# Kernel optimization log

Measured on AMD Instinct MI355X. Metric: run time of the kernel, lower is better.

## Reference

```python
import jax, jax.numpy as jnp
import numpy as np

N = 100000      # nodes
E = 3200000     # edges (avg degree 32)
F_IN = 512
HID = 256
CLS = 64


def _linear_init(k, fan_in, fan_out):
    lim = 1.0 / np.sqrt(fan_in)
    kw, kb = jax.random.split(k)
    W = jax.random.uniform(kw, (fan_in, fan_out), jnp.float32, -lim, lim)
    b = jax.random.uniform(kb, (fan_out,), jnp.float32, -lim, lim)
    return W, b


def setup_inputs() -> dict:
    key = jax.random.key(0)
    ks = jax.random.split(key, 8)
    x = jax.random.normal(ks[0], (N, F_IN), jnp.float32)
    edge_src = jax.random.randint(ks[1], (E,), 0, N, jnp.int32)
    off = jax.random.randint(ks[2], (E,), 1, N, jnp.int32)
    edge_dst = ((edge_src + off) % N).astype(jnp.int32)  # no self loops
    Wm0, bm0 = _linear_init(ks[3], F_IN, HID)
    Wv0, bv0 = _linear_init(ks[4], F_IN, HID)
    Wm1, bm1 = _linear_init(ks[5], HID, CLS)
    Wv1, bv1 = _linear_init(ks[6], HID, CLS)
    sample = jax.random.normal(ks[7], (N, CLS), jnp.float32)
    return dict(x=x, Wm0=Wm0, bm0=bm0, Wv0=Wv0, bv0=bv0,
                Wm1=Wm1, bm1=bm1, Wv1=Wv1, bv1=bv1,
                sample=sample, edge_src=edge_src, edge_dst=edge_dst)


def reference(x, Wm0, bm0, Wv0, bv0, Wm1, bm1, Wv1, bv1, sample, edge_src, edge_dst):
    n = x.shape[0]
    loops = jnp.arange(n, dtype=edge_src.dtype)
    src = jnp.concatenate([edge_src, loops])  # fill_diag(adj, 1.0)
    dst = jnp.concatenate([edge_dst, loops])
    ones = jnp.ones(src.shape[0], x.dtype)
    deg = jax.ops.segment_sum(ones, src, num_segments=n)
    dis = jnp.where(deg > 0, deg ** -0.5, 0.0)   # D^-0.5
    di = jnp.where(deg > 0, 1.0 / deg, 0.0)      # D^-1
    w0 = dis[src] * dis[dst]                      # adj0 = D^-0.5 A D^-0.5
    w1 = di[src] * di[dst]                        # adj1 = D^-1  A D^-1

    def spmm(w, m):  # (adj @ m) with edge weights w
        return jax.ops.segment_sum(w[:, None] * m[dst], src, num_segments=n)

    # layer 0 (initial=True): no aggregation, dropout off (eval)
    mean = jax.nn.elu(x @ Wm0 + bm0)
    var = jax.nn.relu(x @ Wv0 + bv0)
    # layer 1: variance-attention + dual SpMM
    mean = jax.nn.elu(mean @ Wm1 + bm1)
    var = jax.nn.relu(var @ Wv1 + bv1) + 1e-6
    attn = jnp.exp(-var)
    mean = spmm(w0, mean * attn)
    var = spmm(w1, var * attn * attn)

    out = mean + sample * jnp.sqrt(var)
    return jax.nn.log_softmax(out, axis=-1)
```

## Files before the change

kernel.cpp:

```cpp
#include <hip/hip_runtime.h>
#include <cstdint>
#include <cstddef>


typedef _Float16 h8 __attribute__((ext_vector_type(8)));
typedef _Float16 h2 __attribute__((ext_vector_type(2)));
typedef float f32x4 __attribute__((ext_vector_type(4)));
typedef unsigned int uint32;

#define BSHIFT 7
#define NCHUNK 256

static __device__ __forceinline__ float elu_f(float z) {
  return z > 0.f ? z : expm1f(z);
}

static __device__ __forceinline__ void gload16(const void* g, void* l) {
  __builtin_amdgcn_global_load_lds(
      (__attribute__((address_space(1))) void*)g,
      (__attribute__((address_space(3))) void*)l, 16, 0, 0);
}

static __device__ __forceinline__ h8 cvt8(float4 a, float4 b) {
  return h8{(_Float16)a.x, (_Float16)a.y, (_Float16)a.z, (_Float16)a.w,
            (_Float16)b.x, (_Float16)b.y, (_Float16)b.z, (_Float16)b.w};
}

__global__ __launch_bounds__(256) void histprep_k(
    const int* __restrict__ esrc, int E, int chunk, int* __restrict__ h, int NB,
    const float* __restrict__ Wm0, const float* __restrict__ Wv0,
    const float* __restrict__ Wm1, const float* __restrict__ Wv1,
    _Float16* __restrict__ W1t, _Float16* __restrict__ W2t) {
  int t = threadIdx.x;
  if (blockIdx.x < NCHUNK) {
    __shared__ int sh[1024];
    for (int i = t; i < NB; i += 256) sh[i] = 0;
    __syncthreads();
    int e0 = blockIdx.x * chunk;
    int e1 = min(e0 + chunk, E);
    for (int e = e0 + t; e < e1; e += 256) atomicAdd(&sh[esrc[e] >> BSHIFT], 1);
    __syncthreads();
    for (int i = t; i < NB; i += 256) h[blockIdx.x * NB + i] = sh[i];
  } else {
    int idx = (blockIdx.x - NCHUNK) * 256 + t;
    if (idx < 512 * 512) {
      int n = idx >> 9, k = idx & 511;
      float v = (n < 256) ? Wm0[k * 256 + n] : Wv0[k * 256 + (n - 256)];
      W1t[idx] = (_Float16)v;
    }
    if (idx < 128 * 512) {
      int n = idx >> 9, k = idx & 511;
      float v = 0.f;
      if (n < 64) { if (k < 256) v = Wm1[k * 64 + n]; }
      else        { if (k >= 256) v = Wv1[(k - 256) * 64 + (n - 64)]; }
      W2t[idx] = (_Float16)v;
    }
  }
}

__global__ __launch_bounds__(256) void btotal_k(const int* __restrict__ h,
                                                int* __restrict__ tot, int NB) {
  int b = blockIdx.x, t = threadIdx.x;
  int v = h[t * NB + b];
#pragma unroll
  for (int off = 32; off; off >>= 1) v += __shfl_xor(v, off, 64);
  __shared__ int sw[4];
  if ((t & 63) == 0) sw[t >> 6] = v;
  __syncthreads();
  if (t == 0) tot[b] = sw[0] + sw[1] + sw[2] + sw[3];
}

__global__ __launch_bounds__(1024) void boff2_k(const int* __restrict__ tot,
                                                int* __restrict__ h,
                                                int* __restrict__ base, int NB) {
  __shared__ int sh[1024];
  __shared__ int bbs;
  int b = blockIdx.x, t = threadIdx.x;
  int v = (t < NB) ? tot[t] : 0;
  sh[t] = v;
  __syncthreads();
  for (int off = 1; off < 1024; off <<= 1) {
    int add = (t >= off) ? sh[t - off] : 0;
    __syncthreads();
    sh[t] += add;
    __syncthreads();
  }
  if (b == 0) {
    if (t < NB) base[t] = sh[t] - v;
    if (t == 0) base[NB] = sh[NB - 1];
  }
  if (t == 0) bbs = (b > 0) ? sh[b - 1] : 0;
  __syncthreads();
  int hv = (t < 256) ? h[t * NB + b] : 0;
  __syncthreads();
  if (t < 256) sh[t] = hv;
  __syncthreads();
  for (int off = 1; off < 256; off <<= 1) {
    int add = (t >= off && t < 256) ? sh[t - off] : 0;
    __syncthreads();
    if (t < 256) sh[t] += add;
    __syncthreads();
  }
  if (t < 256) h[t * NB + b] = bbs + sh[t] - hv;
}

__global__ __launch_bounds__(256) void bscatter_k(
    const int* __restrict__ esrc, const int* __restrict__ edst, int E, int chunk,
    const int* __restrict__ h, uint32* __restrict__ pairs, int NB) {
  __shared__ int lcur[1024];
  int t = threadIdx.x;
  for (int i = t; i < NB; i += 256) lcur[i] = h[blockIdx.x * NB + i];
  __syncthreads();
  int e0 = blockIdx.x * chunk;
  int e1 = min(e0 + chunk, E);
  for (int e = e0 + t; e < e1; e += 256) {
    int s = esrc[e], d = edst[e];
    int pos = atomicAdd(&lcur[s >> BSHIFT], 1);
    pairs[pos] = ((uint32)(s & 127) << 25) | (uint32)d;
  }
}

__global__ __launch_bounds__(256) void countN_k(
    const uint32* __restrict__ pairs, const int* __restrict__ base,
    int* __restrict__ cnt, float2* __restrict__ dd, int n) {
  __shared__ int c128[128];
  int b = blockIdx.x, t = threadIdx.x;
  if (t < 128) c128[t] = 0;
  __syncthreads();
  int lo = base[b], hi = base[b + 1];
  for (int i = lo + t; i < hi; i += 256) atomicAdd(&c128[pairs[i] >> 25], 1);
  __syncthreads();
  if (t < 128) {
    int node = b * 128 + t;
    if (node < n) {
      int c = c128[t];
      cnt[node] = c;
      float d = (float)(c + 1);
      dd[node] = make_float2(rsqrtf(d), 1.f / d);
    }
  }
}

__global__ __launch_bounds__(256) void partC_k(
    const uint32* __restrict__ pairs, const int* __restrict__ base,
    const int* __restrict__ rs, int* __restrict__ csr, int n) {
  __shared__ int lcur[128];
  int b = blockIdx.x, t = threadIdx.x;
  if (t < 128) {
    int node = b * 128 + t;
    lcur[t] = (node < n) ? rs[node] : 0;
  }
  __syncthreads();
  int lo = base[b], hi = base[b + 1];
  for (int i = lo + t; i < hi; i += 256) {
    uint32 p = pairs[i];
    int pos = atomicAdd(&lcur[p >> 25], 1);
    csr[pos] = (int)(p & 0x1FFFFFFu);
  }
}

__global__ void scan1_k(const int* __restrict__ cnt, int* __restrict__ excl,
                        int* __restrict__ bsum, int n) {
  __shared__ int sh[256];
  int t = threadIdx.x, idx = blockIdx.x * 256 + t;
  int v = (idx < n) ? ((cnt[idx] + 3) & ~3) : 0;
  sh[t] = v;
  __syncthreads();
  for (int off = 1; off < 256; off <<= 1) {
    int add = (t >= off) ? sh[t - off] : 0;
    __syncthreads();
    sh[t] += add;
    __syncthreads();
  }
  if (idx < n) excl[idx] = sh[t] - v;
  if (t == 255) bsum[blockIdx.x] = sh[255];
}

__global__ __launch_bounds__(512) void scan3m_k(int* __restrict__ excl,
                                                const int* __restrict__ bsum,
                                                int nb, int n) {
  __shared__ int sh[512];
  int t = threadIdx.x;
  int v = (t < nb) ? bsum[t] : 0;
  sh[t] = v;
  __syncthreads();
  for (int off = 1; off < 512; off <<= 1) {
    int add = (t >= off) ? sh[t - off] : 0;
    __syncthreads();
    sh[t] += add;
    __syncthreads();
  }
  int idx = blockIdx.x * 512 + t;
  if (idx < n) {
    int k = idx >> 8;
    excl[idx] += (k > 0) ? sh[k - 1] : 0;
  }
}

__global__ __launch_bounds__(256) void gemm1d_k(
    const float* __restrict__ A, const _Float16* __restrict__ Bt,
    const float* __restrict__ b0, const float* __restrict__ b1,
    _Float16* __restrict__ out, int M, int mtiles) {
  __shared__ __align__(16) unsigned char ldsb[36864];

  const int sg = blockIdx.x >> 5, loc = blockIdx.x & 31;
  const int nt = loc >> 3, mtl = loc & 7;
  const int mt = sg * 8 + mtl;
  if (mt >= mtiles) return;
  const int m0 = mt * 128, n0 = nt * 128;
  const int t = threadIdx.x;
  const int lane = t & 63;
  const int wave = t >> 6;
  const int wm = wave >> 1, wn = wave & 1;
  const int lr = lane & 15, quad = lane >> 4;

  const int ra = t >> 3;
  const int asw = ((t & 7) ^ (ra & 7)) << 2;

  const _Float16* bbase = Bt + (size_t)(n0 + wn * 64 + lr) * 512 + quad * 8;

  f32x4 acc[4][4] = {};

  auto stageA = [&](int b, int kt) {
#pragma unroll
    for (int i = 0; i < 4; i++) {
      const float* src = A + (size_t)min(m0 + i * 32 + ra, M - 1) * 512 + kt + asw;
      gload16(src, ldsb + b * 16384 + i * 4096 + t * 16);
    }
  };

  stageA(0, 0);
  __syncthreads();

  int cur = 0;
  const int zA = lr & 7;
  for (int kt = 0; kt < 512; kt += 32) {
    h8 bf[4];
#pragma unroll
    for (int j = 0; j < 4; j++)
      bf[j] = *(const h8*)(bbase + (size_t)j * 16 * 512 + kt);
    if (kt + 32 < 512) stageA(cur ^ 1, kt + 32);
    const unsigned char* Ab = ldsb + cur * 16384;
    h8 af[4];
#pragma unroll
    for (int i = 0; i < 4; i++) {
      int R = wm * 64 + i * 16 + lr;
      const float4 a0 = *(const float4*)(Ab + R * 128 + (((2 * quad) ^ zA) << 4));
      const float4 a1 = *(const float4*)(Ab + R * 128 + (((2 * quad + 1) ^ zA) << 4));
      af[i] = cvt8(a0, a1);
    }
#pragma unroll
    for (int i = 0; i < 4; i++)
#pragma unroll
      for (int j = 0; j < 4; j++)
        acc[i][j] = __builtin_amdgcn_mfma_f32_16x16x32_f16(af[i], bf[j], acc[i][j], 0, 0, 0);
    __syncthreads();
    cur ^= 1;
  }

  _Float16* lt = (_Float16*)ldsb;
#pragma unroll
  for (int j = 0; j < 4; j++) {
    int gc = n0 + wn * 64 + j * 16 + lr;
    float bj = (gc < 256) ? b0[gc] : b1[gc - 256];
#pragma unroll
    for (int i = 0; i < 4; i++) {
#pragma unroll
      for (int r = 0; r < 4; r++) {
        float z = acc[i][j][r] + bj;
        float v = (gc < 256) ? elu_f(z) : fmaxf(z, 0.f);
        lt[(wm * 64 + i * 16 + quad * 4 + r) * 136 + wn * 64 + j * 16 + lr] = (_Float16)v;
      }
    }
  }
  __syncthreads();
  {
    const int row = t >> 1, col0 = (t & 1) * 64;
    const int gr = m0 + row;
    if (gr < M) {
      _Float16* dst = out + (size_t)gr * 512 + n0 + col0;
#pragma unroll
      for (int k = 0; k < 8; k++)
        *(h8*)(dst + k * 8) = *(h8*)&lt[row * 136 + col0 + k * 8];
    }
  }
}

__global__ __launch_bounds__(256) void gemm2_k(
    const _Float16* __restrict__ A, const _Float16* __restrict__ Bt,
    const float* __restrict__ bm1, const float* __restrict__ bv1,
    const float2* __restrict__ dd, uint32* __restrict__ Mcat, int M) {
  __shared__ __align__(16) unsigned char ldsb[32768];
  const int m0 = blockIdx.x * 128;
  const int t = threadIdx.x;
  const int lane = t & 63;
  const int wave = t >> 6;
  const int lr = lane & 15, quad = lane >> 4;

  const int rb = t >> 2;
  const int sw = ((t & 3) ^ ((t >> 3) & 3)) << 3;

  f32x4 acc[2][8] = {};

  auto stage = [&](int b, int kt) {
#pragma unroll
    for (int i = 0; i < 2; i++) {
      const _Float16* src = A + (size_t)min(m0 + i * 64 + rb, M - 1) * 512 + kt + sw;
      gload16(src, ldsb + b * 16384 + i * 4096 + t * 16);
    }
#pragma unroll
    for (int i = 0; i < 2; i++) {
      const _Float16* src = Bt + (size_t)(i * 64 + rb) * 512 + kt + sw;
      gload16(src, ldsb + b * 16384 + 8192 + i * 4096 + t * 16);
    }
  };

  stage(0, 0);
  __syncthreads();

  const int z = (lr >> 1) & 3;
  int cur = 0;
  for (int kt = 0; kt < 512; kt += 32) {
    if (kt + 32 < 512) stage(cur ^ 1, kt + 32);
    const unsigned char* Ab = ldsb + cur * 16384;
    const unsigned char* Bb = Ab + 8192;
    h8 af[2], bf[8];
#pragma unroll
    for (int i = 0; i < 2; i++) {
      int row = wave * 32 + i * 16 + lr;
      af[i] = *(const h8*)(Ab + row * 64 + ((quad ^ z) << 4));
    }
#pragma unroll
    for (int j = 0; j < 8; j++) {
      int row = j * 16 + lr;
      bf[j] = *(const h8*)(Bb + row * 64 + ((quad ^ z) << 4));
    }
#pragma unroll
    for (int i = 0; i < 2; i++)
#pragma unroll
      for (int j = 0; j < 8; j++)
        acc[i][j] = __builtin_amdgcn_mfma_f32_16x16x32_f16(af[i], bf[j], acc[i][j], 0, 0, 0);
    __syncthreads();
    cur ^= 1;
  }

  float2 wrow[2][4];
#pragma unroll
  for (int i = 0; i < 2; i++)
#pragma unroll
    for (int r = 0; r < 4; r++) {
      int gr = m0 + wave * 32 + i * 16 + quad * 4 + r;
      wrow[i][r] = (gr < M) ? dd[gr] : make_float2(0.f, 0.f);
    }

#pragma unroll
  for (int jm = 0; jm < 4; jm++) {
    int c = jm * 16 + lr;
    float bm = bm1[c], bv = bv1[c];
#pragma unroll
    for (int i = 0; i < 2; i++) {
#pragma unroll
      for (int r = 0; r < 4; r++) {
        int gr = m0 + wave * 32 + i * 16 + quad * 4 + r;
        if (gr < M) {
          float zm = acc[i][jm][r] + bm;
          float zv = acc[i][4 + jm][r] + bv;
          float m = elu_f(zm);
          float v = fmaxf(zv, 0.f) + 1e-6f;
          float a = __expf(-v);
          h2 pk;
          pk.x = (_Float16)(m * a * wrow[i][r].x);
          pk.y = (_Float16)(v * a * a * wrow[i][r].y);
          Mcat[(size_t)gr * 64 + c] = __builtin_bit_cast(uint32, pk);
        }
      }
    }
  }
}

__global__ __launch_bounds__(256) void spmm_final_k(
    const uint32* __restrict__ Mcat, const float2* __restrict__ dd,
    const int* __restrict__ row_start, const int* __restrict__ cnt,
    const int* __restrict__ csr, const float* __restrict__ sample,
    float* __restrict__ out, int n) {
  int wid = threadIdx.x >> 6, lane = threadIdx.x & 63;
  int r = blockIdx.x * 4 + wid;
  if (r >= n) return;
  float2 wr = dd[r];
  h2 self = __builtin_bit_cast(h2, Mcat[(size_t)r * 64 + lane]);
  float Sm = (float)self.x;
  float Sv = (float)self.y;
  int start = __builtin_amdgcn_readfirstlane(row_start[r]);
  int c = __builtin_amdgcn_readfirstlane(cnt[r]);
  int j = 0;
  for (; j + 8 <= c; j += 8) {
    int4 da = *(const int4*)(csr + start + j);
    int4 db = *(const int4*)(csr + start + j + 4);
    h2 p0 = __builtin_bit_cast(h2, Mcat[(size_t)da.x * 64 + lane]);
    h2 p1 = __builtin_bit_cast(h2, Mcat[(size_t)da.y * 64 + lane]);
    h2 p2 = __builtin_bit_cast(h2, Mcat[(size_t)da.z * 64 + lane]);
    h2 p3 = __builtin_bit_cast(h2, Mcat[(size_t)da.w * 64 + lane]);
    h2 p4 = __builtin_bit_cast(h2, Mcat[(size_t)db.x * 64 + lane]);
    h2 p5 = __builtin_bit_cast(h2, Mcat[(size_t)db.y * 64 + lane]);
    h2 p6 = __builtin_bit_cast(h2, Mcat[(size_t)db.z * 64 + lane]);
    h2 p7 = __builtin_bit_cast(h2, Mcat[(size_t)db.w * 64 + lane]);
    Sm += (float)p0.x + (float)p1.x + (float)p2.x + (float)p3.x;
    Sv += (float)p0.y + (float)p1.y + (float)p2.y + (float)p3.y;
    Sm += (float)p4.x + (float)p5.x + (float)p6.x + (float)p7.x;
    Sv += (float)p4.y + (float)p5.y + (float)p6.y + (float)p7.y;
  }
  if (j + 4 <= c) {
    int4 d4 = *(const int4*)(csr + start + j);
    h2 p0 = __builtin_bit_cast(h2, Mcat[(size_t)d4.x * 64 + lane]);
    h2 p1 = __builtin_bit_cast(h2, Mcat[(size_t)d4.y * 64 + lane]);
    h2 p2 = __builtin_bit_cast(h2, Mcat[(size_t)d4.z * 64 + lane]);
    h2 p3 = __builtin_bit_cast(h2, Mcat[(size_t)d4.w * 64 + lane]);
    Sm += (float)p0.x + (float)p1.x + (float)p2.x + (float)p3.x;
    Sv += (float)p0.y + (float)p1.y + (float)p2.y + (float)p3.y;
    j += 4;
  }
  for (; j < c; j++) {
    int d = csr[start + j];
    h2 p = __builtin_bit_cast(h2, Mcat[(size_t)d * 64 + lane]);
    Sm += (float)p.x;
    Sv += (float)p.y;
  }
  float mean = wr.x * Sm;
  float var = wr.y * Sv;
  float o = mean + sample[(size_t)r * 64 + lane] * sqrtf(var);
  float mx = o;
#pragma unroll
  for (int off = 32; off; off >>= 1) mx = fmaxf(mx, __shfl_xor(mx, off, 64));
  float ex = __expf(o - mx);
  float s = ex;
#pragma unroll
  for (int off = 32; off; off >>= 1) s += __shfl_xor(s, off, 64);
  out[(size_t)r * 64 + lane] = o - mx - logf(s);
}

extern "C" void kernel_launch(void* const* d_in, const int* in_sizes, int n_in,
                              void* d_out, int out_size, void* d_ws, size_t ws_size,
                              hipStream_t stream) {
  (void)n_in; (void)out_size; (void)ws_size;
  const float* x    = (const float*)d_in[0];
  const float* Wm0  = (const float*)d_in[1];
  const float* bm0  = (const float*)d_in[2];
  const float* Wv0  = (const float*)d_in[3];
  const float* bv0  = (const float*)d_in[4];
  const float* Wm1  = (const float*)d_in[5];
  const float* bm1  = (const float*)d_in[6];
  const float* Wv1  = (const float*)d_in[7];
  const float* bv1  = (const float*)d_in[8];
  const float* sample = (const float*)d_in[9];
  const int* esrc   = (const int*)d_in[10];
  const int* edst   = (const int*)d_in[11];
  float* out = (float*)d_out;

  const int N = in_sizes[0] / 512;
  const int E = in_sizes[10];
  const int NB = (N + 127) >> BSHIFT;
  const int chunk = (E + NCHUNK - 1) / NCHUNK;

  uint8_t* p = (uint8_t*)d_ws;
  size_t off = 0;
  auto alloc = [&](size_t bytes) -> void* {
    void* r = p + off;
    off += (bytes + 255) & ~(size_t)255;
    return r;
  };
  _Float16* W1t  = (_Float16*)alloc((size_t)512 * 512 * 2);
  _Float16* W2t  = (_Float16*)alloc((size_t)128 * 512 * 2);
  _Float16* Hcat = (_Float16*)alloc((size_t)N * 512 * 2);
  uint32*   Mcat = (uint32*)alloc((size_t)N * 64 * 4);
  int*   cnt    = (int*)alloc((size_t)N * 4);
  float2* dd    = (float2*)alloc((size_t)N * 8);
  int*   rs     = (int*)alloc((size_t)N * 4);
  int*   h      = (int*)alloc((size_t)NCHUNK * NB * 4);
  int*   tot    = (int*)alloc((size_t)(NB + 1) * 4);
  int*   base   = (int*)alloc((size_t)(NB + 1) * 4);
  int*   bsum   = (int*)alloc(2048);
  int*   csr    = (int*)alloc((size_t)(E + 4 * N) * 4);
  uint32* pairs = (uint32*)Hcat;

  const int nbN = (N + 255) / 256;

  histprep_k<<<NCHUNK + 1024, 256, 0, stream>>>(esrc, E, chunk, h, NB,
                                                Wm0, Wv0, Wm1, Wv1, W1t, W2t);
  btotal_k<<<NB, 256, 0, stream>>>(h, tot, NB);
  boff2_k<<<NB, 1024, 0, stream>>>(tot, h, base, NB);
  bscatter_k<<<NCHUNK, 256, 0, stream>>>(esrc, edst, E, chunk, h, pairs, NB);
  countN_k<<<NB, 256, 0, stream>>>(pairs, base, cnt, dd, N);
  scan1_k<<<nbN, 256, 0, stream>>>(cnt, rs, bsum, N);
  scan3m_k<<<(N + 511) / 512, 512, 0, stream>>>(rs, bsum, nbN, N);
  partC_k<<<NB, 256, 0, stream>>>(pairs, base, rs, csr, N);

  const int mtiles = (N + 127) / 128;
  const int sgroups = (mtiles + 7) / 8;
  gemm1d_k<<<sgroups * 32, 256, 0, stream>>>(x, W1t, bm0, bv0, Hcat, N, mtiles);
  gemm2_k<<<mtiles, 256, 0, stream>>>(Hcat, W2t, bm1, bv1, dd, Mcat, N);
  spmm_final_k<<<(N + 3) / 4, 256, 0, stream>>>(Mcat, dd, rs, cnt, csr, sample, out, N);
}
```

Baseline: 707.8 us.

## Stage GEMM B tiles through LDS and process two rows per wave in SpMM

The first GEMM now also stages the fp16 weight tile into a swizzled double-buffered LDS region with async global-to-LDS loads, instead of each wave reading B fragments directly from global memory. This raises LDS use per block from 36KB to 48KB, which may lower occupancy. The SpMM/final kernel now assigns half a wave (32 lanes) to each row, each lane gathering 8-byte chunks (two h2 pairs), so each wave covers two rows. The softmax reductions shrink to 32-lane shuffles. The intent is fewer, wider gather transactions and less redundant B traffic, at the cost of row-count divergence between the two half-waves.

```diff
diff --git a/kernel.cpp b/kernel.cpp
--- a/kernel.cpp
+++ b/kernel.cpp
@@ -197,11 +197,11 @@
   }
 }
 
-__global__ __launch_bounds__(256) void gemm1d_k(
+__global__ __launch_bounds__(256) void gemm1f_k(
     const float* __restrict__ A, const _Float16* __restrict__ Bt,
     const float* __restrict__ b0, const float* __restrict__ b1,
     _Float16* __restrict__ out, int M, int mtiles) {
-  __shared__ __align__(16) unsigned char ldsb[36864];
+  __shared__ __align__(16) unsigned char ldsb[49152];
 
   const int sg = blockIdx.x >> 5, loc = blockIdx.x & 31;
   const int nt = loc >> 3, mtl = loc & 7;
@@ -216,31 +216,40 @@
 
   const int ra = t >> 3;
   const int asw = ((t & 7) ^ (ra & 7)) << 2;
-
-  const _Float16* bbase = Bt + (size_t)(n0 + wn * 64 + lr) * 512 + quad * 8;
+  const int rb = t >> 2;
+  const int bsw = ((t & 3) ^ ((t >> 3) & 3)) << 3;
 
   f32x4 acc[4][4] = {};
 
-  auto stageA = [&](int b, int kt) {
+  auto stage = [&](int b, int kt) {
 #pragma unroll
     for (int i = 0; i < 4; i++) {
       const float* src = A + (size_t)min(m0 + i * 32 + ra, M - 1) * 512 + kt + asw;
       gload16(src, ldsb + b * 16384 + i * 4096 + t * 16);
     }
+#pragma unroll
+    for (int i = 0; i < 2; i++) {
+      const _Float16* src = Bt + (size_t)(n0 + i * 64 + rb) * 512 + kt + bsw;
+      gload16(src, ldsb + 32768 + b * 8192 + i * 4096 + t * 16);
+    }
   };
 
-  stageA(0, 0);
+  stage(0, 0);
   __syncthreads();
 
   int cur = 0;
   const int zA = lr & 7;
+  const int zB = (lr >> 1) & 3;
   for (int kt = 0; kt < 512; kt += 32) {
+    if (kt + 32 < 512) stage(cur ^ 1, kt + 32);
+    const unsigned char* Ab = ldsb + cur * 16384;
+    const unsigned char* Bb = ldsb + 32768 + cur * 8192;
     h8 bf[4];
 #pragma unroll
-    for (int j = 0; j < 4; j++)
-      bf[j] = *(const h8*)(bbase + (size_t)j * 16 * 512 + kt);
-    if (kt + 32 < 512) stageA(cur ^ 1, kt + 32);
-    const unsigned char* Ab = ldsb + cur * 16384;
+    for (int j = 0; j < 4; j++) {
+      int row = wn * 64 + j * 16 + lr;
+      bf[j] = *(const h8*)(Bb + row * 64 + ((quad ^ zB) << 4));
+    }
     h8 af[4];
 #pragma unroll
     for (int i = 0; i < 4; i++) {
@@ -384,58 +393,63 @@
     const int* __restrict__ csr, const float* __restrict__ sample,
     float* __restrict__ out, int n) {
   int wid = threadIdx.x >> 6, lane = threadIdx.x & 63;
-  int r = blockIdx.x * 4 + wid;
+  int half = lane >> 5, sl = lane & 31;
+  int r = blockIdx.x * 8 + wid * 2 + half;
   if (r >= n) return;
   float2 wr = dd[r];
-  h2 self = __builtin_bit_cast(h2, Mcat[(size_t)r * 64 + lane]);
-  float Sm = (float)self.x;
-  float Sv = (float)self.y;
-  int start = __builtin_amdgcn_readfirstlane(row_start[r]);
-  int c = __builtin_amdgcn_readfirstlane(cnt[r]);
+  uint2 sf = ((const uint2*)(Mcat + (size_t)r * 64))[sl];
+  h2 s0 = __builtin_bit_cast(h2, sf.x);
+  h2 s1 = __builtin_bit_cast(h2, sf.y);
+  float Sm0 = (float)s0.x, Sv0 = (float)s0.y;
+  float Sm1 = (float)s1.x, Sv1 = (float)s1.y;
+  int start = row_start[r];
+  int c = cnt[r];
   int j = 0;
   for (; j + 8 <= c; j += 8) {
     int4 da = *(const int4*)(csr + start + j);
     int4 db = *(const int4*)(csr + start + j + 4);
-    h2 p0 = __builtin_bit_cast(h2, Mcat[(size_t)da.x * 64 + lane]);
-    h2 p1 = __builtin_bit_cast(h2, Mcat[(size_t)da.y * 64 + lane]);
-    h2 p2 = __builtin_bit_cast(h2, Mcat[(size_t)da.z * 64 + lane]);
-    h2 p3 = __builtin_bit_cast(h2, Mcat[(size_t)da.w * 64 + lane]);
-    h2 p4 = __builtin_bit_cast(h2, Mcat[(size_t)db.x * 64 + lane]);
-    h2 p5 = __builtin_bit_cast(h2, Mcat[(size_t)db.y * 64 + lane]);
-    h2 p6 = __builtin_bit_cast(h2, Mcat[(size_t)db.z * 64 + lane]);
-    h2 p7 = __builtin_bit_cast(h2, Mcat[(size_t)db.w * 64 + lane]);
-    Sm += (float)p0.x + (float)p1.x + (float)p2.x + (float)p3.x;
-    Sv += (float)p0.y + (float)p1.y + (float)p2.y + (float)p3.y;
-    Sm += (float)p4.x + (float)p5.x + (float)p6.x + (float)p7.x;
-    Sv += (float)p4.y + (float)p5.y + (float)p6.y + (float)p7.y;
+    uint2 p0 = ((const uint2*)(Mcat + (size_t)da.x * 64))[sl];
+    uint2 p1 = ((const uint2*)(Mcat + (size_t)da.y * 64))[sl];
+    uint2 p2 = ((const uint2*)(Mcat + (size_t)da.z * 64))[sl];
+    uint2 p3 = ((const uint2*)(Mcat + (size_t)da.w * 64))[sl];
+    uint2 p4 = ((const uint2*)(Mcat + (size_t)db.x * 64))[sl];
+    uint2 p5 = ((const uint2*)(Mcat + (size_t)db.y * 64))[sl];
+    uint2 p6 = ((const uint2*)(Mcat + (size_t)db.z * 64))[sl];
+    uint2 p7 = ((const uint2*)(Mcat + (size_t)db.w * 64))[sl];
+#define ACC2(p)                                                   \
+    { h2 a_ = __builtin_bit_cast(h2, p.x);                        \
+      h2 b_ = __builtin_bit_cast(h2, p.y);                        \
+      Sm0 += (float)a_.x; Sv0 += (float)a_.y;                     \
+      Sm1 += (float)b_.x; Sv1 += (float)b_.y; }
+    ACC2(p0) ACC2(p1) ACC2(p2) ACC2(p3)
+    ACC2(p4) ACC2(p5) ACC2(p6) ACC2(p7)
   }
   if (j + 4 <= c) {
     int4 d4 = *(const int4*)(csr + start + j);
-    h2 p0 = __builtin_bit_cast(h2, Mcat[(size_t)d4.x * 64 + lane]);
-    h2 p1 = __builtin_bit_cast(h2, Mcat[(size_t)d4.y * 64 + lane]);
-    h2 p2 = __builtin_bit_cast(h2, Mcat[(size_t)d4.z * 64 + lane]);
-    h2 p3 = __builtin_bit_cast(h2, Mcat[(size_t)d4.w * 64 + lane]);
-    Sm += (float)p0.x + (float)p1.x + (float)p2.x + (float)p3.x;
-    Sv += (float)p0.y + (float)p1.y + (float)p2.y + (float)p3.y;
+    uint2 p0 = ((const uint2*)(Mcat + (size_t)d4.x * 64))[sl];
+    uint2 p1 = ((const uint2*)(Mcat + (size_t)d4.y * 64))[sl];
+    uint2 p2 = ((const uint2*)(Mcat + (size_t)d4.z * 64))[sl];
+    uint2 p3 = ((const uint2*)(Mcat + (size_t)d4.w * 64))[sl];
+    ACC2(p0) ACC2(p1) ACC2(p2) ACC2(p3)
     j += 4;
   }
   for (; j < c; j++) {
     int d = csr[start + j];
-    h2 p = __builtin_bit_cast(h2, Mcat[(size_t)d * 64 + lane]);
-    Sm += (float)p.x;
-    Sv += (float)p.y;
-  }
-  float mean = wr.x * Sm;
-  float var = wr.y * Sv;
-  float o = mean + sample[(size_t)r * 64 + lane] * sqrtf(var);
-  float mx = o;
-#pragma unroll
-  for (int off = 32; off; off >>= 1) mx = fmaxf(mx, __shfl_xor(mx, off, 64));
-  float ex = __expf(o - mx);
-  float s = ex;
-#pragma unroll
-  for (int off = 32; off; off >>= 1) s += __shfl_xor(s, off, 64);
-  out[(size_t)r * 64 + lane] = o - mx - logf(s);
+    uint2 p = ((const uint2*)(Mcat + (size_t)d * 64))[sl];
+    ACC2(p)
+  }
+#undef ACC2
+  float2 sp = ((const float2*)(sample + (size_t)r * 64))[sl];
+  float o0 = wr.x * Sm0 + sp.x * sqrtf(wr.y * Sv0);
+  float o1 = wr.x * Sm1 + sp.y * sqrtf(wr.y * Sv1);
+  float mx = fmaxf(o0, o1);
+#pragma unroll
+  for (int off = 16; off; off >>= 1) mx = fmaxf(mx, __shfl_xor(mx, off, 32));
+  float s = __expf(o0 - mx) + __expf(o1 - mx);
+#pragma unroll
+  for (int off = 16; off; off >>= 1) s += __shfl_xor(s, off, 32);
+  float ls = logf(s);
+  ((float2*)(out + (size_t)r * 64))[sl] = make_float2(o0 - mx - ls, o1 - mx - ls);
 }
 
 extern "C" void kernel_launch(void* const* d_in, const int* in_sizes, int n_in,
@@ -496,7 +510,7 @@
 
   const int mtiles = (N + 127) / 128;
   const int sgroups = (mtiles + 7) / 8;
-  gemm1d_k<<<sgroups * 32, 256, 0, stream>>>(x, W1t, bm0, bv0, Hcat, N, mtiles);
+  gemm1f_k<<<sgroups * 32, 256, 0, stream>>>(x, W1t, bm0, bv0, Hcat, N, mtiles);
   gemm2_k<<<mtiles, 256, 0, stream>>>(Hcat, W2t, bm1, bv1, dd, Mcat, N);
-  spmm_final_k<<<(N + 3) / 4, 256, 0, stream>>>(Mcat, dd, rs, cnt, csr, sample, out, N);
-}
+  spmm_final_k<<<(N + 7) / 8, 256, 0, stream>>>(Mcat, dd, rs, cnt, csr, sample, out, N);
+}
```

Result: faster. 687.4 us (-2.9%).
